# Performance work log

Measured on AMD Instinct MI355X. Metric: run time of the kernel, lower is better.

## Reference

```python
import jax, jax.numpy as jnp
import numpy as np

B, T, C = 2, 2048, 2048
H, D = 16, 128  # num_heads, head_dim


def setup_inputs() -> dict:
    key = jax.random.key(0)
    ks = jax.random.split(key, 5)
    x = jax.random.normal(ks[0], (B, T, C), dtype=jnp.float32)
    # causal mask: mask==0 positions are filled with -inf
    mask = jnp.tril(jnp.ones((T, T), dtype=jnp.int32))[None, None, :, :]
    wq = jax.random.normal(ks[1], (C, C), dtype=jnp.float32) * (C ** -0.5)
    wk = jax.random.normal(ks[2], (C, C), dtype=jnp.float32) * (C ** -0.5)
    wv = jax.random.normal(ks[3], (C, C), dtype=jnp.float32) * (C ** -0.5)
    wo = jax.random.normal(ks[4], (C, C), dtype=jnp.float32) * (C ** -0.5)
    return {"x": x, "mask": mask, "wq": wq, "wk": wk, "wv": wv, "wo": wo}


def reference(x, mask, wq, wk, wv, wo):
    Bx, Tx, Cx = x.shape
    scale = D ** -0.5
    # torch Linear: y = x @ W.T (weights are [out, in])
    q = (x @ wq.T).reshape(Bx, Tx, H, D).transpose(0, 2, 1, 3)  # [B,H,T,D]
    k = (x @ wk.T).reshape(Bx, Tx, H, D).transpose(0, 2, 1, 3)
    v = (x @ wv.T).reshape(Bx, Tx, H, D).transpose(0, 2, 1, 3)
    scores = jnp.einsum("bhqd,bhkd->bhqk", q, k) * scale  # [B,H,T,T]
    scores = jnp.where(mask == 0, -jnp.inf, scores)
    attn = jax.nn.softmax(scores, axis=-1)
    out = jnp.einsum("bhqk,bhkd->bhqd", attn, v)  # [B,H,T,D]
    out = out.transpose(0, 2, 1, 3).reshape(Bx, Tx, Cx)
    return out @ wo.T
```

## Files before the change

kernel.cpp:

```cpp
#include <hip/hip_runtime.h>
#include <hip/hip_bf16.h>


#define BB 2
#define TT 2048
#define CC 2048
#define HH 16
#define DD 128
#define MM (BB*TT)
#define NQT (TT/64)
#define GNT (CC/64)

typedef __bf16 bf16x8 __attribute__((ext_vector_type(8)));
typedef __bf16 bf16x4 __attribute__((ext_vector_type(4)));
typedef float  f32x4  __attribute__((ext_vector_type(4)));

#define MFMA16(a, b, c) __builtin_amdgcn_mfma_f32_16x16x32_bf16((a), (b), (c), 0, 0, 0)

__device__ __forceinline__ void g2lds16(const void* g, void* l) {
    __builtin_amdgcn_global_load_lds(
        (const __attribute__((address_space(1))) void*)g,
        (__attribute__((address_space(3))) void*)l,
        16, 0, 0);
}

__global__ __launch_bounds__(256) void cvt_all(
    const float* __restrict__ x,  const float* __restrict__ wq,
    const float* __restrict__ wk, const float* __restrict__ wv,
    const float* __restrict__ wo, __bf16* __restrict__ out_base)
{
    const int idx = blockIdx.x * 256 + threadIdx.x;
    const float* in; int off;
    if (idx < (1 << 21)) { in = x; off = idx; }
    else {
        const int r = idx - (1 << 21);
        const int k = r >> 20;
        in  = (k == 0) ? wq : (k == 1) ? wk : (k == 2) ? wv : wo;
        off = r & ((1 << 20) - 1);
    }
    const float4 v = ((const float4*)in)[off];
    bf16x4 o;
    o.x = (__bf16)v.x; o.y = (__bf16)v.y;
    o.z = (__bf16)v.z; o.w = (__bf16)v.w;
    ((bf16x4*)out_base)[idx] = o;
}

__global__ __launch_bounds__(512, 2) void gemm_qk(
    const __bf16* __restrict__ A, const __bf16* __restrict__ Wt,
    __bf16* __restrict__ out)
{
    __shared__ __align__(16) __bf16 As[2][256*64];
    __shared__ __align__(16) __bf16 Bs[2][2][256*32];

    const int tid = threadIdx.x;
    const int w   = tid >> 6, lane = tid & 63;
    const int wm  = w >> 2,  wn  = w & 3;
    const int lo  = lane & 15, hi = lane >> 4;
    const int xr  = (lo & 7) << 4;
    const int xb2 = ((lo >> 1) & 3) << 4;

    const int bid = blockIdx.y * gridDim.x + blockIdx.x;
    const int xcd = bid & 7, loc = bid >> 3;
    const int n0  = (2*xcd + (loc & 1)) * 256;
    const int m0  = (loc >> 1) * 256;

    const int ar   = tid >> 3, as_ = tid & 7;
    const int acol = ((as_ ^ (ar & 7)) << 3);
    const int brr  = tid >> 2, bs_ = tid & 3;
    const int bcol = ((bs_ ^ ((brr >> 1) & 3)) << 3);

    auto stageA = [&](int buf, int kt) {
        #pragma unroll
        for (int j = 0; j < 4; ++j)
            g2lds16(A + (size_t)(m0 + j*64 + ar)*CC + kt*64 + acol,
                    (char*)&As[buf][0] + j*8192 + w*1024);
    };
    auto stageB = [&](int buf, int kt) {
        #pragma unroll
        for (int ks = 0; ks < 2; ++ks)
            #pragma unroll
            for (int jb = 0; jb < 2; ++jb)
                g2lds16(Wt + (size_t)(n0 + jb*128 + brr)*CC + kt*64 + ks*32 + bcol,
                        (char*)&Bs[buf][ks][0] + jb*8192 + w*1024);
    };
    auto rdA = [&](bf16x8* af, int buf, int ks) {
        const char* base = (const char*)&As[buf][0];
        #pragma unroll
        for (int mf = 0; mf < 8; ++mf) {
            const int r = wm*128 + mf*16 + lo;
            af[mf] = *(const bf16x8*)(base + r*128 + ((ks*64 + hi*16) ^ xr));
        }
    };
    auto rdB = [&](bf16x8* bv, int buf, int ks) {
        const char* base = (const char*)&Bs[buf][ks][0];
        #pragma unroll
        for (int nf = 0; nf < 4; ++nf) {
            const int n = wn*64 + nf*16 + lo;
            bv[nf] = *(const bf16x8*)(base + n*64 + ((hi*16) ^ xb2));
        }
    };

    f32x4 acc[8][4] = {};

    stageA(0, 0); stageB(0, 0);
    asm volatile("s_waitcnt vmcnt(0)" ::: "memory");
    __builtin_amdgcn_s_barrier();

    int buf = 0;
    #pragma unroll 1
    for (int t = 0; t < GNT; ++t) {
        const bool hn = (t + 1 < GNT);
        {
            bf16x8 af[8], bv[4];
            rdA(af, buf, 0); rdB(bv, buf, 0);
            if (hn) stageA(buf ^ 1, t + 1);
            __builtin_amdgcn_s_setprio(1);
            #pragma unroll
            for (int mf = 0; mf < 8; ++mf)
                #pragma unroll
                for (int nf = 0; nf < 4; ++nf)
                    acc[mf][nf] = MFMA16(af[mf], bv[nf], acc[mf][nf]);
            __builtin_amdgcn_s_setprio(0);
        }
        {
            bf16x8 af[8], bv[4];
            rdA(af, buf, 1); rdB(bv, buf, 1);
            if (hn) stageB(buf ^ 1, t + 1);
            __builtin_amdgcn_s_setprio(1);
            #pragma unroll
            for (int mf = 0; mf < 8; ++mf)
                #pragma unroll
                for (int nf = 0; nf < 4; ++nf)
                    acc[mf][nf] = MFMA16(af[mf], bv[nf], acc[mf][nf]);
            __builtin_amdgcn_s_setprio(0);
            if (hn) {
                asm volatile("s_waitcnt vmcnt(0)" ::: "memory");
                __builtin_amdgcn_s_barrier();
            }
        }
        buf ^= 1;
    }

    #pragma unroll
    for (int mf = 0; mf < 8; ++mf) {
        #pragma unroll
        for (int nf = 0; nf < 4; ++nf) {
            #pragma unroll
            for (int r = 0; r < 4; ++r) {
                const int row = m0 + wm*128 + mf*16 + hi*4 + r;
                const int col = n0 + wn*64 + nf*16 + lo;
                const int seg = col >> 11;
                const int c2  = col & (CC-1);
                const int b = row >> 11, t_ = row & (TT-1);
                const int h = c2 >> 7,  d  = c2 & (DD-1);
                __bf16* dst = out + (size_t)seg * MM * CC;
                dst[(size_t)((b*HH + h)*TT + t_)*DD + d] = (__bf16)acc[mf][nf][r];
            }
        }
    }
}

template<int MODE>
__global__ __launch_bounds__(512, 2) void gemm_bt(
    const __bf16* __restrict__ A, const __bf16* __restrict__ Wt,
    void* __restrict__ out)
{
    __shared__ __align__(16) __bf16 As[3][256*64];
    __shared__ __align__(16) __bf16 Bs[3][2][128*32];

    const int tid = threadIdx.x;
    const int w   = tid >> 6, lane = tid & 63;
    const int wm  = w >> 1,  wn  = w & 1;
    const int lo  = lane & 15, hi = lane >> 4;
    const int xr  = (lo & 7) << 4;
    const int xb2 = ((lo >> 1) & 3) << 4;

    const int bid   = blockIdx.y * gridDim.x + blockIdx.x;
    const int xcd   = bid & 7, loc = bid >> 3;
    const int n0    = (2*xcd + (loc & 1)) * 128;
    const int m0    = (loc >> 1) * 256;

    const int ar   = tid >> 3, as_ = tid & 7;
    const int acol = ((as_ ^ (ar & 7)) << 3);
    const int br   = tid >> 2, bs_ = tid & 3;
    const int bcol = ((bs_ ^ ((br >> 1) & 3)) << 3);

    auto stageA3a = [&](int buf, int kt) {
        #pragma unroll
        for (int j = 0; j < 3; ++j)
            g2lds16(A + (size_t)(m0 + j*64 + ar)*CC + kt*64 + acol,
                    (char*)&As[buf][0] + j*8192 + w*1024);
    };
    auto stageA3b = [&](int buf, int kt) {
        g2lds16(A + (size_t)(m0 + 3*64 + ar)*CC + kt*64 + acol,
                (char*)&As[buf][0] + 3*8192 + w*1024);
        #pragma unroll
        for (int kh = 0; kh < 2; ++kh)
            g2lds16(Wt + (size_t)(n0 + br)*CC + kt*64 + kh*32 + bcol,
                    (char*)&Bs[buf][kh][0] + w*1024);
    };
    auto rdA = [&](bf16x8* af, int buf, int ks) {
        const char* base = (const char*)&As[buf][0];
        #pragma unroll
        for (int mf = 0; mf < 4; ++mf) {
            const int r = wm*64 + mf*16 + lo;
            af[mf] = *(const bf16x8*)(base + r*128 + ((ks*64 + hi*16) ^ xr));
        }
    };
    auto rdB = [&](bf16x8* bv, int buf, int ks) {
        const char* base = (const char*)&Bs[buf][ks][0];
        #pragma unroll
        for (int nf = 0; nf < 4; ++nf) {
            const int n = wn*64 + nf*16 + lo;
            bv[nf] = *(const bf16x8*)(base + n*64 + ((hi*16) ^ xb2));
        }
    };

    f32x4 acc[4][4] = {};

    stageA3a(0, 0); stageA3b(0, 0);
    stageA3a(1, 1); stageA3b(1, 1);
    asm volatile("s_waitcnt vmcnt(6)" ::: "memory");
    __builtin_amdgcn_s_barrier();

    int rb = 0;
    #pragma unroll 1
    for (int t = 0; t < GNT - 2; ++t) {
        const int sb = (rb == 0) ? 2 : rb - 1;
        {
            bf16x8 af[4], bv[4];
            rdA(af, rb, 0); rdB(bv, rb, 0);
            stageA3a(sb, t + 2);
            __builtin_amdgcn_s_setprio(1);
            #pragma unroll
            for (int mf = 0; mf < 4; ++mf)
                #pragma unroll
                for (int nf = 0; nf < 4; ++nf)
                    acc[mf][nf] = MFMA16(af[mf], bv[nf], acc[mf][nf]);
            __builtin_amdgcn_s_setprio(0);
        }
        {
            bf16x8 af[4], bv[4];
            rdA(af, rb, 1); rdB(bv, rb, 1);
            stageA3b(sb, t + 2);
            __builtin_amdgcn_s_setprio(1);
            #pragma unroll
            for (int mf = 0; mf < 4; ++mf)
                #pragma unroll
                for (int nf = 0; nf < 4; ++nf)
                    acc[mf][nf] = MFMA16(af[mf], bv[nf], acc[mf][nf]);
            __builtin_amdgcn_s_setprio(0);
            asm volatile("s_waitcnt vmcnt(6)" ::: "memory");
            __builtin_amdgcn_s_barrier();
        }
        rb = (rb == 2) ? 0 : rb + 1;
    }
    {
        bf16x8 af[4], bv[4];
        rdA(af, rb, 0); rdB(bv, rb, 0);
        #pragma unroll
        for (int mf = 0; mf < 4; ++mf)
            #pragma unroll
            for (int nf = 0; nf < 4; ++nf)
                acc[mf][nf] = MFMA16(af[mf], bv[nf], acc[mf][nf]);
        rdA(af, rb, 1); rdB(bv, rb, 1);
        #pragma unroll
        for (int mf = 0; mf < 4; ++mf)
            #pragma unroll
            for (int nf = 0; nf < 4; ++nf)
                acc[mf][nf] = MFMA16(af[mf], bv[nf], acc[mf][nf]);
        asm volatile("s_waitcnt vmcnt(0)" ::: "memory");
        __builtin_amdgcn_s_barrier();
        rb = (rb == 2) ? 0 : rb + 1;
    }
    {
        bf16x8 af[4], bv[4];
        rdA(af, rb, 0); rdB(bv, rb, 0);
        #pragma unroll
        for (int mf = 0; mf < 4; ++mf)
            #pragma unroll
            for (int nf = 0; nf < 4; ++nf)
                acc[mf][nf] = MFMA16(af[mf], bv[nf], acc[mf][nf]);
        rdA(af, rb, 1); rdB(bv, rb, 1);
        #pragma unroll
        for (int mf = 0; mf < 4; ++mf)
            #pragma unroll
            for (int nf = 0; nf < 4; ++nf)
                acc[mf][nf] = MFMA16(af[mf], bv[nf], acc[mf][nf]);
    }

    #pragma unroll
    for (int mf = 0; mf < 4; ++mf) {
        #pragma unroll
        for (int nf = 0; nf < 4; ++nf) {
            #pragma unroll
            for (int r = 0; r < 4; ++r) {
                const int row = m0 + wm*64 + mf*16 + hi*4 + r;
                const int col = n0 + wn*64 + nf*16 + lo;
                const float v = acc[mf][nf][r];
                if (MODE == 1) {
                    const int b = row >> 11, t = row & (TT-1);
                    const int h = col >> 7,  d = col & (DD-1);
                    ((__bf16*)out)[(size_t)((b*HH + h)*DD + d)*TT + t] = (__bf16)v;
                } else {
                    ((float*)out)[(size_t)row*CC + col] = v;
                }
            }
        }
    }
}

__global__ __launch_bounds__(256, 2) void attn_fwd(
    const __bf16* __restrict__ Q, const __bf16* __restrict__ K,
    const __bf16* __restrict__ Vt, __bf16* __restrict__ O)
{
    __shared__ __align__(16) __bf16 Ks[2][64*128];
    __shared__ __align__(16) __bf16 Vs[2][128*64];
    __shared__ __align__(16) __bf16 Ps[4][16*64];

    const int lid   = blockIdx.y * gridDim.x + blockIdx.x;
    const int bh    = lid & 31;
    const int pairx = lid >> 5;
    const int tid = threadIdx.x;
    const int w   = tid >> 6, lane = tid & 63;
    const int lo  = lane & 15, hi = lane >> 4;
    const int xr  = (lo & 7) << 4;

    const int krow_l  = lane >> 4;
    const int kcol_sw = ((lane & 15) << 4);
    const int vrow_l  = lane >> 3;
    const int vcol_sw = (((lane & 7) ^ (lane >> 3)) << 3);

    const size_t kbase = (size_t)bh * TT * DD;
    const size_t vbase = (size_t)bh * DD * TT;
    const int b = bh >> 4, h = bh & 15;
    const float SC = 0.12754613142f;

    bf16x8 vones;
    #pragma unroll
    for (int i = 0; i < 8; ++i) vones[i] = (__bf16)1.0f;

    auto stage = [&](int buf, int kv0) {
        #pragma unroll
        for (int i = 0; i < 4; ++i) {
            const int c = 4*w + i;
            {
                const int row = 4*c + krow_l;
                const int sw  = (kcol_sw ^ ((row & 7) << 4)) >> 1;
                g2lds16(K + kbase + (size_t)(kv0 + row)*DD + sw,
                        &Ks[buf][0] + c*512);
            }
            {
                const int row = 8*c + vrow_l;
                g2lds16(Vt + vbase + (size_t)row*TT + kv0 + vcol_sw,
                        &Vs[buf][0] + c*512);
            }
        }
    };

    #pragma unroll 1
    for (int half = 0; half < 2; ++half) {
        const int qt = half ? pairx : (NQT - 1 - pairx);
        const int q0 = qt * 64;

        const __bf16* Qbase = Q + (kbase + (size_t)(q0 + w*16 + lo) * DD);
        bf16x8 qf[4];
        #pragma unroll
        for (int kc = 0; kc < 4; ++kc)
            qf[kc] = *(const bf16x8*)(Qbase + kc*32 + hi*8);

        float mrow[4];
        #pragma unroll
        for (int r = 0; r < 4; ++r) mrow[r] = -1e30f;
        f32x4 oacc[8] = {};
        f32x4 sacc = {};

        const int qg_base = q0 + w*16 + hi*4;
        const int ntiles  = qt + 1;

        stage(0, 0);
        __syncthreads();
        int cur = 0;

        for (int t = 0; t < ntiles; ++t) {
            const int kv0 = t*64;
            if (t + 1 < ntiles) stage(cur ^ 1, (t+1)*64);

            const char* Kb = (const char*)&Ks[cur][0];
            const char* Vb = (const char*)&Vs[cur][0];

            f32x4 s[4];
            __builtin_amdgcn_s_setprio(1);
            #pragma unroll
            for (int st = 0; st < 4; ++st) {
                f32x4 a = {};
                #pragma unroll
                for (int kc = 0; kc < 4; ++kc) {
                    const bf16x8 kf = *(const bf16x8*)(
                        Kb + (st*16 + lo)*256 + ((kc*64 + hi*16) ^ xr));
                    a = MFMA16(qf[kc], kf, a);
                }
                s[st] = a;
            }
            __builtin_amdgcn_s_setprio(0);

            float pmax[4];
            const bool diag = (t == ntiles - 1);
            #pragma unroll
            for (int r = 0; r < 4; ++r) {
                const int qg = qg_base + r;
                float mx = -1e30f;
                #pragma unroll
                for (int st = 0; st < 4; ++st) {
                    float v = s[st][r] * SC;
                    if (diag) {
                        const int kvg = kv0 + st*16 + lo;
                        v = (kvg > qg) ? -1e30f : v;
                    }
                    s[st][r] = v;
                    mx = fmaxf(mx, v);
                }
                #pragma unroll
                for (int msk = 1; msk < 16; msk <<= 1)
                    mx = fmaxf(mx, __shfl_xor(mx, msk, 64));
                pmax[r] = mx;
            }

            bool need = false;
            #pragma unroll
            for (int r = 0; r < 4; ++r)
                need = need || (pmax[r] > mrow[r] + 11.5f);
            if (__any(need)) {
                float rsc[4];
                #pragma unroll
                for (int r = 0; r < 4; ++r) {
                    const float mnew = fmaxf(mrow[r], pmax[r]);
                    rsc[r]  = __builtin_amdgcn_exp2f(mrow[r] - mnew);
                    mrow[r] = mnew;
                    sacc[r] *= rsc[r];
                }
                #pragma unroll
                for (int dc = 0; dc < 8; ++dc)
                    #pragma unroll
                    for (int r = 0; r < 4; ++r)
                        oacc[dc][r] *= rsc[r];
            }

            #pragma unroll
            for (int r = 0; r < 4; ++r)
                #pragma unroll
                for (int st = 0; st < 4; ++st)
                    s[st][r] = __builtin_amdgcn_exp2f(s[st][r] - mrow[r]);

            char* Pw = (char*)&Ps[w][0];
            #pragma unroll
            for (int st = 0; st < 4; ++st)
                #pragma unroll
                for (int r = 0; r < 4; ++r) {
                    const int row = hi*4 + r;
                    *(__bf16*)(Pw + row*128 + (((st*16 + lo)*2) ^ ((row & 7) << 4)))
                        = (__bf16)s[st][r];
                }

            __builtin_amdgcn_s_setprio(1);
            #pragma unroll
            for (int kc2 = 0; kc2 < 2; ++kc2) {
                const bf16x8 pf = *(const bf16x8*)(
                    Pw + lo*128 + ((kc2*64 + hi*16) ^ xr));
                #pragma unroll
                for (int dc = 0; dc < 8; ++dc) {
                    const bf16x8 vf = *(const bf16x8*)(
                        Vb + (dc*16 + lo)*128 + ((kc2*64 + hi*16) ^ xr));
                    oacc[dc] = MFMA16(pf, vf, oacc[dc]);
                }
                sacc = MFMA16(pf, vones, sacc);
            }
            __builtin_amdgcn_s_setprio(0);

            __syncthreads();
            cur ^= 1;
        }

        #pragma unroll
        for (int r = 0; r < 4; ++r) {
            const float inv = 1.f / sacc[r];
            const int qg = qg_base + r;
            #pragma unroll
            for (int dc = 0; dc < 8; ++dc) {
                const int d = dc*16 + lo;
                O[(size_t)(b*TT + qg)*CC + h*DD + d] = (__bf16)(oacc[dc][r] * inv);
            }
        }
    }
}

extern "C" void kernel_launch(void* const* d_in, const int* in_sizes, int n_in,
                              void* d_out, int out_size, void* d_ws, size_t ws_size,
                              hipStream_t stream) {
    const float* x  = (const float*)d_in[0];
    const float* wq = (const float*)d_in[2];
    const float* wk = (const float*)d_in[3];
    const float* wv = (const float*)d_in[4];
    const float* wo = (const float*)d_in[5];

    char* p = (char*)d_ws;
    __bf16* xb  = (__bf16*)p; p += (size_t)MM*CC*2;
    __bf16* wqb = (__bf16*)p; p += (size_t)CC*CC*2;
    __bf16* wkb = (__bf16*)p; p += (size_t)CC*CC*2;
    __bf16* wvb = (__bf16*)p; p += (size_t)CC*CC*2;
    __bf16* wob = (__bf16*)p; p += (size_t)CC*CC*2;
    __bf16* Qb  = (__bf16*)p; p += (size_t)MM*CC*2;
    __bf16* Kb  = (__bf16*)p; p += (size_t)MM*CC*2;
    __bf16* Vtb = (__bf16*)p; p += (size_t)MM*CC*2;
    __bf16* AOb = xb;
    (void)wkb;

    cvt_all<<<24576, 256, 0, stream>>>(x, wq, wk, wv, wo, xb);

    gemm_qk<<<dim3(16, 16), 512, 0, stream>>>(xb, wqb, Qb);
    gemm_bt<1><<<dim3(16, 16), 512, 0, stream>>>(xb, wvb, Vtb);

    attn_fwd<<<dim3(NQT/2, BB*HH), 256, 0, stream>>>(Qb, Kb, Vtb, AOb);

    gemm_bt<2><<<dim3(16, 16), 512, 0, stream>>>(AOb, wob, (void*)d_out);
}
```

Measured before the change: 222.2 us.

## Transpose QK^T MFMA so each lane owns one query row for softmax

The QK^T MFMA operands are swapped so the score tile comes out transposed, with each lane holding one query row's scores. This turns the per-row max into mostly in-register work, needing only two cross-lane shuffles, and keeps a single running max per lane instead of four. The rescale factors are then shuffled back into the output-accumulator layout. P is written to LDS as packed 8-byte stores instead of sixteen scalar bf16 stores. The cost is extra shuffles when the rescale branch fires, and the masking and swizzle indexing must stay consistent with the new layout.

Measured after the change: 208.2 us. 1.07x faster.

```diff
diff --git a/kernel.cpp b/kernel.cpp
--- a/kernel.cpp
+++ b/kernel.cpp
@@ -1,5 +1,6 @@
 #include <hip/hip_runtime.h>
 #include <hip/hip_bf16.h>
+#include <string.h>
 
 
 #define BB 2
@@ -22,6 +23,13 @@
         (const __attribute__((address_space(1))) void*)g,
         (__attribute__((address_space(3))) void*)l,
         16, 0, 0);
+}
+
+__device__ __forceinline__ unsigned pack_bf16x2(float a, float b) {
+    __bf16 ba = (__bf16)a, bb = (__bf16)b;
+    unsigned short ua, ub;
+    memcpy(&ua, &ba, 2); memcpy(&ub, &bb, 2);
+    return (unsigned)ua | ((unsigned)ub << 16);
 }
 
 __global__ __launch_bounds__(256) void cvt_all(
@@ -369,12 +377,11 @@
         for (int kc = 0; kc < 4; ++kc)
             qf[kc] = *(const bf16x8*)(Qbase + kc*32 + hi*8);
 
-        float mrow[4];
-        #pragma unroll
-        for (int r = 0; r < 4; ++r) mrow[r] = -1e30f;
+        float mrow = -1e30f;
         f32x4 oacc[8] = {};
         f32x4 sacc = {};
 
+        const int qg_lane = q0 + w*16 + lo;
         const int qg_base = q0 + w*16 + hi*4;
         const int ntiles  = qt + 1;
 
@@ -398,69 +405,62 @@
                 for (int kc = 0; kc < 4; ++kc) {
                     const bf16x8 kf = *(const bf16x8*)(
                         Kb + (st*16 + lo)*256 + ((kc*64 + hi*16) ^ xr));
-                    a = MFMA16(qf[kc], kf, a);
+                    a = MFMA16(kf, qf[kc], a);
                 }
                 s[st] = a;
             }
             __builtin_amdgcn_s_setprio(0);
 
-            float pmax[4];
+            float lmax = -1e30f;
             const bool diag = (t == ntiles - 1);
             #pragma unroll
-            for (int r = 0; r < 4; ++r) {
-                const int qg = qg_base + r;
-                float mx = -1e30f;
-                #pragma unroll
-                for (int st = 0; st < 4; ++st) {
+            for (int st = 0; st < 4; ++st) {
+                #pragma unroll
+                for (int r = 0; r < 4; ++r) {
                     float v = s[st][r] * SC;
                     if (diag) {
-                        const int kvg = kv0 + st*16 + lo;
-                        v = (kvg > qg) ? -1e30f : v;
+                        const int kvg = kv0 + st*16 + hi*4 + r;
+                        v = (kvg > qg_lane) ? -1e30f : v;
                     }
                     s[st][r] = v;
-                    mx = fmaxf(mx, v);
+                    lmax = fmaxf(lmax, v);
                 }
-                #pragma unroll
-                for (int msk = 1; msk < 16; msk <<= 1)
-                    mx = fmaxf(mx, __shfl_xor(mx, msk, 64));
-                pmax[r] = mx;
-            }
-
-            bool need = false;
-            #pragma unroll
-            for (int r = 0; r < 4; ++r)
-                need = need || (pmax[r] > mrow[r] + 11.5f);
-            if (__any(need)) {
-                float rsc[4];
-                #pragma unroll
-                for (int r = 0; r < 4; ++r) {
-                    const float mnew = fmaxf(mrow[r], pmax[r]);
-                    rsc[r]  = __builtin_amdgcn_exp2f(mrow[r] - mnew);
-                    mrow[r] = mnew;
-                    sacc[r] *= rsc[r];
-                }
+            }
+
+            if (__any(lmax > mrow + 11.5f)) {
+                float mx = lmax;
+                mx = fmaxf(mx, __shfl_xor(mx, 16, 64));
+                mx = fmaxf(mx, __shfl_xor(mx, 32, 64));
+                const float mnew = fmaxf(mrow, mx);
+                const float rsc  = __builtin_amdgcn_exp2f(mrow - mnew);
+                mrow = mnew;
+                float rscO[4];
+                #pragma unroll
+                for (int r = 0; r < 4; ++r)
+                    rscO[r] = __shfl(rsc, (lane & 48) | (hi*4 + r), 64);
+                #pragma unroll
+                for (int r = 0; r < 4; ++r) sacc[r] *= rscO[r];
                 #pragma unroll
                 for (int dc = 0; dc < 8; ++dc)
                     #pragma unroll
                     for (int r = 0; r < 4; ++r)
-                        oacc[dc][r] *= rsc[r];
-            }
-
-            #pragma unroll
-            for (int r = 0; r < 4; ++r)
-                #pragma unroll
-                for (int st = 0; st < 4; ++st)
-                    s[st][r] = __builtin_amdgcn_exp2f(s[st][r] - mrow[r]);
+                        oacc[dc][r] *= rscO[r];
+            }
+
+            #pragma unroll
+            for (int st = 0; st < 4; ++st)
+                #pragma unroll
+                for (int r = 0; r < 4; ++r)
+                    s[st][r] = __builtin_amdgcn_exp2f(s[st][r] - mrow);
 
             char* Pw = (char*)&Ps[w][0];
             #pragma unroll
-            for (int st = 0; st < 4; ++st)
-                #pragma unroll
-                for (int r = 0; r < 4; ++r) {
-                    const int row = hi*4 + r;
-                    *(__bf16*)(Pw + row*128 + (((st*16 + lo)*2) ^ ((row & 7) << 4)))
-                        = (__bf16)s[st][r];
-                }
+            for (int st = 0; st < 4; ++st) {
+                uint2 dw;
+                dw.x = pack_bf16x2(s[st][0], s[st][1]);
+                dw.y = pack_bf16x2(s[st][2], s[st][3]);
+                *(uint2*)(Pw + lo*128 + ((st*32 + hi*8) ^ xr)) = dw;
+            }
 
             __builtin_amdgcn_s_setprio(1);
             #pragma unroll
```
